# Kernel optimization log

Measured on AMD Instinct MI355X. Metric: run time of the kernel, lower is better.

The kernel has to match this reference:

```python
import jax, jax.numpy as jnp
import numpy as np

DIM = 256
NUM_HEADS = 8
HEAD_DIM = DIM // NUM_HEADS


def setup_inputs() -> dict:
    key = jax.random.key(0)
    k_x, k_wq, k_bq, k_wp, k_bp = jax.random.split(key, 5)
    x = jax.random.normal(k_x, (4, DIM, 64, 64), dtype=jnp.float32)
    # 1x1 convs == per-pixel linear layers over channels
    w_qkv = jax.random.normal(k_wq, (3 * DIM, DIM), dtype=jnp.float32) * (DIM ** -0.5)
    b_qkv = jax.random.normal(k_bq, (3 * DIM,), dtype=jnp.float32) * 0.02
    w_proj = jax.random.normal(k_wp, (DIM, DIM), dtype=jnp.float32) * (DIM ** -0.5)
    b_proj = jax.random.normal(k_bp, (DIM,), dtype=jnp.float32) * 0.02
    return {"x": x, "w_qkv": w_qkv, "b_qkv": b_qkv, "w_proj": w_proj, "b_proj": b_proj}


def reference(x, w_qkv, b_qkv, w_proj, b_proj):
    B, C, H, W = x.shape
    S = H * W
    h, d = NUM_HEADS, HEAD_DIM
    # flatten spatial dims: (B, C, H, W) -> (B, S, C)
    xf = x.reshape(B, C, S).transpose(0, 2, 1)
    # 1x1 conv qkv: (B, S, 3C)
    qkv = xf @ w_qkv.T + b_qkv
    q, k, v = jnp.split(qkv, 3, axis=-1)
    # channel dim splits as (heads, head_dim): (B, S, C) -> (B, h, S, d)
    split = lambda t: t.reshape(B, S, h, d).transpose(0, 2, 1, 3)
    q, k, v = split(q), split(k), split(v)
    scale = d ** -0.5
    attn = jnp.einsum('bhsd,bhtd->bhst', q, k) * scale  # (B, h, S, S)
    attn = jax.nn.softmax(attn, axis=-1)
    out = jnp.einsum('bhst,bhtd->bhsd', attn, v)
    # merge heads: (B, h, S, d) -> (B, S, C)
    out = out.transpose(0, 2, 1, 3).reshape(B, S, C)
    out = out @ w_proj.T + b_proj
    # back to (B, C, H, W)
    return out.transpose(0, 2, 1).reshape(B, C, H, W)
```

## Files before the change

kernel.cpp:

```cpp
#include <hip/hip_runtime.h>


typedef __attribute__((ext_vector_type(8))) short short8;
typedef __attribute__((ext_vector_type(4))) float f4;

__device__ __forceinline__ short f2bs(float f) {
  union { float f; unsigned u; } v; v.f = f;
  unsigned r = v.u + 0x7FFFu + ((v.u >> 16) & 1u);
  return (short)(r >> 16);
}

__device__ __forceinline__ short8 cvt8(f4 a, f4 b) {
  short8 o;
  o[0] = f2bs(a[0]); o[1] = f2bs(a[1]); o[2] = f2bs(a[2]); o[3] = f2bs(a[3]);
  o[4] = f2bs(b[0]); o[5] = f2bs(b[1]); o[6] = f2bs(b[2]); o[7] = f2bs(b[3]);
  return o;
}

__device__ __forceinline__ int pkhu(float lo, float hi) {
  union { float f; unsigned u; } a, b; a.f = lo; b.f = hi;
  return (int)__builtin_amdgcn_perm(b.u + 0x8000u, a.u + 0x8000u, 0x07060302u);
}

__global__ __launch_bounds__(256) void k_qkv(
    const float* __restrict__ x, const float* __restrict__ w,
    const float* __restrict__ bias,
    short* __restrict__ Qr, short* __restrict__ Kq, short* __restrict__ Vt) {
  const int tid = threadIdx.x;
  const int L = tid & 63, wv = tid >> 6;
  const int ln15 = L & 15, quad = L >> 4;
  const int mt = blockIdx.x;
  const int b = mt >> 6;
  const int s0 = (mt & 63) << 6;
  const int j0 = blockIdx.y << 6;
  const int jw = j0 + wv * 16;

  __shared__ __align__(16) short tl[4 * 64 * 16];

  f4 acc[4] = {{0,0,0,0},{0,0,0,0},{0,0,0,0},{0,0,0,0}};
  const float* wb = w + (jw + ln15) * 256 + quad * 8;
  const float* xb = x + b * (256 * 4096) + s0 + ln15;

#pragma unroll 2
  for (int cb = 0; cb < 256; cb += 32) {
    f4 a0 = *(const f4*)(wb + cb);
    f4 a1 = *(const f4*)(wb + cb + 4);
    short8 af = cvt8(a0, a1);
    const float* xc = xb + (cb + quad * 8) * 4096;
#pragma unroll
    for (int sub = 0; sub < 4; ++sub) {
      const float* xs = xc + sub * 16;
      short8 bf;
#pragma unroll
      for (int jj = 0; jj < 8; ++jj) bf[jj] = f2bs(xs[jj * 4096]);
      acc[sub] = __builtin_amdgcn_mfma_f32_16x16x32_bf16(af, bf, acc[sub], 0, 0, 0);
    }
  }

  float bj[4];
#pragma unroll
  for (int r = 0; r < 4; ++r) bj[r] = bias[jw + quad * 4 + r];

  const int type = j0 >> 8;
  if (type == 2) {
    const int jv = jw - 512;
    const int h = jv >> 5;
    const int dbase = jv & 31;
#pragma unroll
    for (int r = 0; r < 4; ++r) {
      const int d = dbase + quad * 4 + r;
      short* vp = Vt + (size_t)((b * 8 + h) * 32 + d) * 4096 + s0 + ln15;
#pragma unroll
      for (int sub = 0; sub < 4; ++sub)
        vp[sub * 16] = f2bs(acc[sub][r] + bj[r]);
    }
  } else {
    const float qsc = 0.17677669529663689f * 1.44269504088896f;
    const float mul = (type == 0) ? qsc : 1.0f;
    short* dst = (type == 0) ? Qr : Kq;
    const int hj = jw & 255;
    short* tw = tl + wv * 1024;
#pragma unroll
    for (int sub = 0; sub < 4; ++sub) {
      const int s = sub * 16 + ln15;
      const int swz = (s >> 2) & 1;
#pragma unroll
      for (int r = 0; r < 4; ++r) {
        const int dl = quad * 4 + r;
        tw[s * 16 + (((dl >> 3) ^ swz) * 8) + (dl & 7)] = f2bs((acc[sub][r] + bj[r]) * mul);
      }
    }
    const int h = hj >> 5;
    const int d0 = hj & 31;
#pragma unroll
    for (int i = 0; i < 2; ++i) {
      const int sl = i * 32 + (L >> 1);
      const int gg = L & 1;
      const int g2 = gg ^ ((sl >> 2) & 1);
      short8 row = *(const short8*)(tw + sl * 16 + g2 * 8);
      *(short8*)(dst + (size_t)((b * 8 + h) * 4096 + s0 + sl) * 32 + d0 + gg * 8) = row;
    }
  }
}

__global__ __launch_bounds__(256, 8) void k_attn(
    const short* __restrict__ Qr, const short* __restrict__ Kq,
    const short* __restrict__ Vt, short* __restrict__ O) {
  const int tid = threadIdx.x;
  const int L = tid & 63, wv = tid >> 6;
  const int ln15 = L & 15, quad = L >> 4;
  const int bh = blockIdx.y;
  const int b = bh >> 3, h = bh & 7;
  const int qt = wv & 1, half = wv >> 1;
  const int qb = blockIdx.x * 64 + qt * 32;

  const short* Qb = Qr + (size_t)bh * 4096 * 32;
  const short* Kb = Kq + (size_t)bh * 4096 * 32 + half * 2048 * 32;
  const short* Vb = Vt + (size_t)bh * 32 * 4096 + half * 2048;

  __shared__ __align__(16) short plds[4][2048];
  __shared__ float l_up[2][32];
  short* pw = plds[wv];
  const int sw = ln15 & 14;

  short8 qf[2];
#pragma unroll
  for (int qs = 0; qs < 2; ++qs)
    qf[qs] = *(const short8*)(Qb + (qb + qs * 16 + ln15) * 32 + quad * 8);

  f4 acc[2][2] = {{{0,0,0,0},{0,0,0,0}},{{0,0,0,0},{0,0,0,0}}};
  float lsum[2] = {0.f, 0.f};
  const f4 z4 = {0.f, 0.f, 0.f, 0.f};

  const short* kp = Kb + ln15 * 32 + quad * 8;
  const short* vp = Vb + ln15 * 4096 + quad * 8;

  for (int kb = 0; kb < 2048; kb += 64) {
#pragma unroll
    for (int t = 0; t < 4; ++t) {
      short8 kf = *(const short8*)(kp + (kb + t * 16) * 32);
#pragma unroll
      for (int qs = 0; qs < 2; ++qs) {
        f4 sc = __builtin_amdgcn_mfma_f32_16x16x32_bf16(kf, qf[qs], z4, 0, 0, 0);
        float p0 = __builtin_amdgcn_exp2f(sc[0]);
        float p1 = __builtin_amdgcn_exp2f(sc[1]);
        float p2 = __builtin_amdgcn_exp2f(sc[2]);
        float p3 = __builtin_amdgcn_exp2f(sc[3]);
        lsum[qs] += (p0 + p1) + (p2 + p3);
        int2 pr;
        pr.x = pkhu(p0, p1);
        pr.y = pkhu(p2, p3);
        const int gw = ((t << 2) + quad) ^ sw;
        *(int2*)(pw + qs * 1024 + ln15 * 64 + gw * 4) = pr;
      }
    }
#pragma unroll
    for (int ks = 0; ks < 2; ++ks) {
      short8 vf0 = *(const short8*)(vp + kb + ks * 32);
      short8 vf1 = *(const short8*)(vp + 16 * 4096 + kb + ks * 32);
#pragma unroll
      for (int qs = 0; qs < 2; ++qs) {
        const int g0 = ((ks << 3) + (quad << 1)) ^ sw;
        short8 pf = *(const short8*)(pw + qs * 1024 + ln15 * 64 + g0 * 4);
        acc[qs][0] = __builtin_amdgcn_mfma_f32_16x16x32_bf16(pf, vf0, acc[qs][0], 0, 0, 0);
        acc[qs][1] = __builtin_amdgcn_mfma_f32_16x16x32_bf16(pf, vf1, acc[qs][1], 0, 0, 0);
      }
    }
  }

  float lfull[2];
#pragma unroll
  for (int qs = 0; qs < 2; ++qs) {
    float l = lsum[qs];
    l += __shfl_xor(l, 16);
    l += __shfl_xor(l, 32);
    lfull[qs] = l;
  }

  if (half == 1) {
    float* cw = (float*)plds[wv];
#pragma unroll
    for (int qs = 0; qs < 2; ++qs) {
#pragma unroll
      for (int dg = 0; dg < 2; ++dg)
#pragma unroll
        for (int r = 0; r < 4; ++r)
          cw[(qs * 16 + quad * 4 + r) * 32 + dg * 16 + ln15] = acc[qs][dg][r];
      if (quad == 0) l_up[qt][qs * 16 + ln15] = lfull[qs];
    }
  }
  __syncthreads();
  if (half == 0) {
    const float* cu = (const float*)plds[wv + 2];
#pragma unroll
    for (int qs = 0; qs < 2; ++qs) {
#pragma unroll
      for (int r = 0; r < 4; ++r) {
        const float lown = __shfl(lfull[qs], quad * 4 + r);
        const float lup = l_up[qt][qs * 16 + quad * 4 + r];
        const float rl = 1.0f / (lown + lup);
        const int sg = qb + qs * 16 + quad * 4 + r;
        short* op = O + (size_t)(b * 4096 + sg) * 256 + h * 32 + ln15;
        const int ci = (qs * 16 + quad * 4 + r) * 32 + ln15;
        op[0]  = f2bs((acc[qs][0][r] + cu[ci]) * rl);
        op[16] = f2bs((acc[qs][1][r] + cu[ci + 16]) * rl);
      }
    }
  }
}

__global__ __launch_bounds__(256) void k_proj(
    const short* __restrict__ O, const float* __restrict__ w,
    const float* __restrict__ bias, float* __restrict__ out) {
  const int tid = threadIdx.x;
  const int L = tid & 63, wv = tid >> 6;
  const int ln15 = L & 15, quad = L >> 4;
  const int m0 = blockIdx.x * 64 + wv * 16;
  const int n0 = blockIdx.y << 6;
  const int b = m0 >> 12, s0 = m0 & 4095;

  f4 acc[4] = {{0,0,0,0},{0,0,0,0},{0,0,0,0},{0,0,0,0}};
  const short* Ob = O + (size_t)(m0 + ln15) * 256 + quad * 8;
  const float* wb = w + (n0 + ln15) * 256 + quad * 8;

#pragma unroll 2
  for (int cb = 0; cb < 256; cb += 32) {
    short8 af = *(const short8*)(Ob + cb);
#pragma unroll
    for (int sub = 0; sub < 4; ++sub) {
      f4 b0 = *(const f4*)(wb + sub * (16 * 256) + cb);
      f4 b1 = *(const f4*)(wb + sub * (16 * 256) + cb + 4);
      short8 bf = cvt8(b0, b1);
      acc[sub] = __builtin_amdgcn_mfma_f32_16x16x32_bf16(af, bf, acc[sub], 0, 0, 0);
    }
  }

  __shared__ float tl[4][64 * 17];
  float* tw = tl[wv];
#pragma unroll
  for (int sub = 0; sub < 4; ++sub) {
    const float bv = bias[n0 + sub * 16 + ln15];
#pragma unroll
    for (int r = 0; r < 4; ++r)
      tw[(sub * 16 + ln15) * 17 + quad * 4 + r] = acc[sub][r] + bv;
  }
#pragma unroll
  for (int i = 0; i < 4; ++i) {
    const int c = i * 16 + (L >> 2);
    const int ms = (L & 3) * 4;
    f4 v;
#pragma unroll
    for (int j = 0; j < 4; ++j) v[j] = tw[c * 17 + ms + j];
    *(f4*)(out + (size_t)b * (256 * 4096) + (size_t)(n0 + c) * 4096 + s0 + ms) = v;
  }
}

extern "C" void kernel_launch(void* const* d_in, const int* in_sizes, int n_in,
                              void* d_out, int out_size, void* d_ws, size_t ws_size,
                              hipStream_t stream) {
  const float* x      = (const float*)d_in[0];
  const float* w_qkv  = (const float*)d_in[1];
  const float* b_qkv  = (const float*)d_in[2];
  const float* w_proj = (const float*)d_in[3];
  const float* b_proj = (const float*)d_in[4];
  float* out = (float*)d_out;

  const size_t SEG = (size_t)4 * 8 * 4096 * 32;
  short* Qr = (short*)d_ws;
  short* Kq = Qr + SEG;
  short* Vt = Kq + SEG;
  short* O  = Vt + SEG;

  k_qkv <<<dim3(256, 12), 256, 0, stream>>>(x, w_qkv, b_qkv, Qr, Kq, Vt);
  k_attn<<<dim3(64, 32),  256, 0, stream>>>(Qr, Kq, Vt, O);
  k_proj<<<dim3(256, 4),  256, 0, stream>>>(O, w_proj, b_proj, out);
}
```

Baseline: 328.0 us.

## Pre-convert weights and transpose x to bf16, prefetch K in attention

Adds two prep kernels: one converts the QKV and projection weights to bf16, the other transposes x into a bf16 (B,S,C) layout through swizzled shared memory. The QKV and projection GEMMs then load contiguous bf16 fragments instead of strided fp32 loads with per-element conversion. The attention loop double-buffers K fragments in registers and lowers launch bounds occupancy from 8 to 6. Epilogues are also rewritten: Q/K are stored directly, V goes through an LDS transpose, and proj writes without LDS. The cost is two extra launches and the O buffer being reused as scratch for the transposed x.

```diff
diff --git a/kernel.cpp b/kernel.cpp
--- a/kernel.cpp
+++ b/kernel.cpp
@@ -10,11 +10,8 @@
   return (short)(r >> 16);
 }
 
-__device__ __forceinline__ short8 cvt8(f4 a, f4 b) {
-  short8 o;
-  o[0] = f2bs(a[0]); o[1] = f2bs(a[1]); o[2] = f2bs(a[2]); o[3] = f2bs(a[3]);
-  o[4] = f2bs(b[0]); o[5] = f2bs(b[1]); o[6] = f2bs(b[2]); o[7] = f2bs(b[3]);
-  return o;
+__device__ __forceinline__ int pkrne(float a, float b) {
+  return (int)((unsigned short)f2bs(a) | ((unsigned)f2bs(b) << 16));
 }
 
 __device__ __forceinline__ int pkhu(float lo, float hi) {
@@ -22,8 +19,47 @@
   return (int)__builtin_amdgcn_perm(b.u + 0x8000u, a.u + 0x8000u, 0x07060302u);
 }
 
+__global__ __launch_bounds__(256) void k_prep_w(
+    const float* __restrict__ wq, const float* __restrict__ wp,
+    short* __restrict__ wqb, short* __restrict__ wpb) {
+  const int i = blockIdx.x * 256 + threadIdx.x;
+  const int NQ = 768 * 256 / 4;
+  f4 v; short* dst; int off;
+  if (i < NQ) { v = ((const f4*)wq)[i]; dst = wqb; off = i * 4; }
+  else        { v = ((const f4*)wp)[i - NQ]; dst = wpb; off = (i - NQ) * 4; }
+  int2 pr; pr.x = pkrne(v[0], v[1]); pr.y = pkrne(v[2], v[3]);
+  *(int2*)(dst + off) = pr;
+}
+
+__global__ __launch_bounds__(256) void k_prep_x(
+    const float* __restrict__ x, short* __restrict__ xT) {
+  const int t = threadIdx.x;
+  const int b = blockIdx.z, c0 = blockIdx.y * 64, s0 = blockIdx.x * 64;
+  __shared__ __align__(16) short tile[64 * 64];
+#pragma unroll
+  for (int pass = 0; pass < 4; ++pass) {
+    const int cl = pass * 16 + (t >> 4);
+    const int sl = (t & 15) * 4;
+    f4 v = *(const f4*)(x + ((size_t)(b * 256 + c0 + cl)) * 4096 + s0 + sl);
+#pragma unroll
+    for (int k = 0; k < 4; ++k) {
+      const int s = sl + k;
+      tile[s * 64 + (cl ^ ((s & 7) << 3))] = f2bs(v[k]);
+    }
+  }
+  __syncthreads();
+#pragma unroll
+  for (int i = 0; i < 2; ++i) {
+    const int s = t >> 2;
+    const int gc = (t & 3) + i * 4;
+    const int gg = gc ^ (s & 7);
+    short8 row = *(const short8*)(tile + s * 64 + gg * 8);
+    *(short8*)(xT + ((size_t)(b * 4096 + s0 + s)) * 256 + c0 + gc * 8) = row;
+  }
+}
+
 __global__ __launch_bounds__(256) void k_qkv(
-    const float* __restrict__ x, const float* __restrict__ w,
+    const short* __restrict__ xT, const short* __restrict__ wqb,
     const float* __restrict__ bias,
     short* __restrict__ Qr, short* __restrict__ Kq, short* __restrict__ Vt) {
   const int tid = threadIdx.x;
@@ -35,75 +71,66 @@
   const int j0 = blockIdx.y << 6;
   const int jw = j0 + wv * 16;
 
-  __shared__ __align__(16) short tl[4 * 64 * 16];
+  __shared__ __align__(16) short tl[4][1024];
 
   f4 acc[4] = {{0,0,0,0},{0,0,0,0},{0,0,0,0},{0,0,0,0}};
-  const float* wb = w + (jw + ln15) * 256 + quad * 8;
-  const float* xb = x + b * (256 * 4096) + s0 + ln15;
-
-#pragma unroll 2
+  const short* wb = wqb + (jw + ln15) * 256 + quad * 8;
+  const short* xb = xT + (size_t)(b * 4096 + s0 + ln15) * 256 + quad * 8;
+
+#pragma unroll
   for (int cb = 0; cb < 256; cb += 32) {
-    f4 a0 = *(const f4*)(wb + cb);
-    f4 a1 = *(const f4*)(wb + cb + 4);
-    short8 af = cvt8(a0, a1);
-    const float* xc = xb + (cb + quad * 8) * 4096;
+    short8 af = *(const short8*)(wb + cb);
 #pragma unroll
     for (int sub = 0; sub < 4; ++sub) {
-      const float* xs = xc + sub * 16;
-      short8 bf;
-#pragma unroll
-      for (int jj = 0; jj < 8; ++jj) bf[jj] = f2bs(xs[jj * 4096]);
-      acc[sub] = __builtin_amdgcn_mfma_f32_16x16x32_bf16(af, bf, acc[sub], 0, 0, 0);
-    }
-  }
-
+      short8 bfr = *(const short8*)(xb + sub * (16 * 256) + cb);
+      acc[sub] = __builtin_amdgcn_mfma_f32_16x16x32_bf16(af, bfr, acc[sub], 0, 0, 0);
+    }
+  }
   float bj[4];
 #pragma unroll
   for (int r = 0; r < 4; ++r) bj[r] = bias[jw + quad * 4 + r];
 
   const int type = j0 >> 8;
-  if (type == 2) {
-    const int jv = jw - 512;
-    const int h = jv >> 5;
-    const int dbase = jv & 31;
-#pragma unroll
-    for (int r = 0; r < 4; ++r) {
-      const int d = dbase + quad * 4 + r;
-      short* vp = Vt + (size_t)((b * 8 + h) * 32 + d) * 4096 + s0 + ln15;
-#pragma unroll
-      for (int sub = 0; sub < 4; ++sub)
-        vp[sub * 16] = f2bs(acc[sub][r] + bj[r]);
-    }
-  } else {
+  const int hj = jw & 255;
+  const int bh = b * 8 + (hj >> 5);
+  const int db = hj & 31;
+
+  if (type != 2) {
     const float qsc = 0.17677669529663689f * 1.44269504088896f;
     const float mul = (type == 0) ? qsc : 1.0f;
     short* dst = (type == 0) ? Qr : Kq;
-    const int hj = jw & 255;
-    short* tw = tl + wv * 1024;
+#pragma unroll
+    for (int sub = 0; sub < 4; ++sub) {
+      float v0 = (acc[sub][0] + bj[0]) * mul;
+      float v1 = (acc[sub][1] + bj[1]) * mul;
+      float v2 = (acc[sub][2] + bj[2]) * mul;
+      float v3 = (acc[sub][3] + bj[3]) * mul;
+      int2 pr; pr.x = pkhu(v0, v1); pr.y = pkhu(v2, v3);
+      *(int2*)(dst + (size_t)(bh * 4096 + s0 + sub * 16 + ln15) * 32 + db + quad * 4) = pr;
+    }
+  } else {
+    short* tv = tl[wv];
 #pragma unroll
     for (int sub = 0; sub < 4; ++sub) {
       const int s = sub * 16 + ln15;
-      const int swz = (s >> 2) & 1;
 #pragma unroll
       for (int r = 0; r < 4; ++r) {
         const int dl = quad * 4 + r;
-        tw[s * 16 + (((dl >> 3) ^ swz) * 8) + (dl & 7)] = f2bs((acc[sub][r] + bj[r]) * mul);
+        tv[dl * 64 + ((((s >> 3) ^ dl) & 7) << 3) + (s & 7)] = f2bs(acc[sub][r] + bj[r]);
       }
     }
-    const int h = hj >> 5;
-    const int d0 = hj & 31;
 #pragma unroll
     for (int i = 0; i < 2; ++i) {
-      const int sl = i * 32 + (L >> 1);
-      const int gg = L & 1;
-      const int g2 = gg ^ ((sl >> 2) & 1);
-      short8 row = *(const short8*)(tw + sl * 16 + g2 * 8);
-      *(short8*)(dst + (size_t)((b * 8 + h) * 4096 + s0 + sl) * 32 + d0 + gg * 8) = row;
-    }
-  }
-}
-
-__global__ __launch_bounds__(256, 8) void k_attn(
+      const int dl = i * 8 + (L >> 3);
+      const int gs = L & 7;
+      const int gg = gs ^ (dl & 7);
+      short8 row = *(const short8*)(tv + dl * 64 + gg * 8);
+      *(short8*)(Vt + (size_t)(bh * 32 + db + dl) * 4096 + s0 + gs * 8) = row;
+    }
+  }
+}
+
+__global__ __launch_bounds__(256, 6) void k_attn(
     const short* __restrict__ Qr, const short* __restrict__ Kq,
     const short* __restrict__ Vt, short* __restrict__ O) {
   const int tid = threadIdx.x;
@@ -135,13 +162,19 @@
   const short* kp = Kb + ln15 * 32 + quad * 8;
   const short* vp = Vb + ln15 * 4096 + quad * 8;
 
-  for (int kb = 0; kb < 2048; kb += 64) {
+  short8 kfA[4], kfB[4];
+#pragma unroll
+  for (int t = 0; t < 4; ++t) kfA[t] = *(const short8*)(kp + t * 16 * 32);
+
+  auto chunk = [&](int kb, short8* kfu, short8* kfn, int knext) {
+#pragma unroll
+    for (int t = 0; t < 4; ++t)
+      kfn[t] = *(const short8*)(kp + (knext + t * 16) * 32);
 #pragma unroll
     for (int t = 0; t < 4; ++t) {
-      short8 kf = *(const short8*)(kp + (kb + t * 16) * 32);
 #pragma unroll
       for (int qs = 0; qs < 2; ++qs) {
-        f4 sc = __builtin_amdgcn_mfma_f32_16x16x32_bf16(kf, qf[qs], z4, 0, 0, 0);
+        f4 sc = __builtin_amdgcn_mfma_f32_16x16x32_bf16(kfu[t], qf[qs], z4, 0, 0, 0);
         float p0 = __builtin_amdgcn_exp2f(sc[0]);
         float p1 = __builtin_amdgcn_exp2f(sc[1]);
         float p2 = __builtin_amdgcn_exp2f(sc[2]);
@@ -166,6 +199,11 @@
         acc[qs][1] = __builtin_amdgcn_mfma_f32_16x16x32_bf16(pf, vf1, acc[qs][1], 0, 0, 0);
       }
     }
+  };
+
+  for (int kb = 0; kb < 2048; kb += 128) {
+    chunk(kb, kfA, kfB, kb + 64);
+    chunk(kb + 64, kfB, kfA, (kb + 128) & 2047);
   }
 
   float lfull[2];
@@ -210,7 +248,7 @@
 }
 
 __global__ __launch_bounds__(256) void k_proj(
-    const short* __restrict__ O, const float* __restrict__ w,
+    const short* __restrict__ O, const short* __restrict__ wpb,
     const float* __restrict__ bias, float* __restrict__ out) {
   const int tid = threadIdx.x;
   const int L = tid & 63, wv = tid >> 6;
@@ -221,37 +259,25 @@
 
   f4 acc[4] = {{0,0,0,0},{0,0,0,0},{0,0,0,0},{0,0,0,0}};
   const short* Ob = O + (size_t)(m0 + ln15) * 256 + quad * 8;
-  const float* wb = w + (n0 + ln15) * 256 + quad * 8;
-
-#pragma unroll 2
+  const short* wb = wpb + (n0 + ln15) * 256 + quad * 8;
+
+#pragma unroll
   for (int cb = 0; cb < 256; cb += 32) {
     short8 af = *(const short8*)(Ob + cb);
 #pragma unroll
     for (int sub = 0; sub < 4; ++sub) {
-      f4 b0 = *(const f4*)(wb + sub * (16 * 256) + cb);
-      f4 b1 = *(const f4*)(wb + sub * (16 * 256) + cb + 4);
-      short8 bf = cvt8(b0, b1);
-      acc[sub] = __builtin_amdgcn_mfma_f32_16x16x32_bf16(af, bf, acc[sub], 0, 0, 0);
-    }
-  }
-
-  __shared__ float tl[4][64 * 17];
-  float* tw = tl[wv];
+      short8 bfr = *(const short8*)(wb + sub * (16 * 256) + cb);
+      acc[sub] = __builtin_amdgcn_mfma_f32_16x16x32_bf16(af, bfr, acc[sub], 0, 0, 0);
+    }
+  }
 #pragma unroll
   for (int sub = 0; sub < 4; ++sub) {
-    const float bv = bias[n0 + sub * 16 + ln15];
-#pragma unroll
-    for (int r = 0; r < 4; ++r)
-      tw[(sub * 16 + ln15) * 17 + quad * 4 + r] = acc[sub][r] + bv;
-  }
-#pragma unroll
-  for (int i = 0; i < 4; ++i) {
-    const int c = i * 16 + (L >> 2);
-    const int ms = (L & 3) * 4;
+    const int c = n0 + sub * 16 + ln15;
+    const float bv = bias[c];
     f4 v;
 #pragma unroll
-    for (int j = 0; j < 4; ++j) v[j] = tw[c * 17 + ms + j];
-    *(f4*)(out + (size_t)b * (256 * 4096) + (size_t)(n0 + c) * 4096 + s0 + ms) = v;
+    for (int r = 0; r < 4; ++r) v[r] = acc[sub][r] + bv;
+    *(f4*)(out + (size_t)b * (256 * 4096) + (size_t)c * 4096 + s0 + quad * 4) = v;
   }
 }
 
@@ -266,12 +292,16 @@
   float* out = (float*)d_out;
 
   const size_t SEG = (size_t)4 * 8 * 4096 * 32;
-  short* Qr = (short*)d_ws;
-  short* Kq = Qr + SEG;
-  short* Vt = Kq + SEG;
-  short* O  = Vt + SEG;
-
-  k_qkv <<<dim3(256, 12), 256, 0, stream>>>(x, w_qkv, b_qkv, Qr, Kq, Vt);
-  k_attn<<<dim3(64, 32),  256, 0, stream>>>(Qr, Kq, Vt, O);
-  k_proj<<<dim3(256, 4),  256, 0, stream>>>(O, w_proj, b_proj, out);
-}
+  short* Qr  = (short*)d_ws;
+  short* Kq  = Qr + SEG;
+  short* Vt  = Kq + SEG;
+  short* OX  = Vt + SEG;
+  short* wqb = OX + SEG;
+  short* wpb = wqb + 768 * 256;
+
+  k_prep_w<<<256, 256, 0, stream>>>(w_qkv, w_proj, wqb, wpb);
+  k_prep_x<<<dim3(64, 4, 4), 256, 0, stream>>>(x, OX);
+  k_qkv <<<dim3(256, 12), 256, 0, stream>>>(OX, wqb, b_qkv, Qr, Kq, Vt);
+  k_attn<<<dim3(64, 32),  256, 0, stream>>>(Qr, Kq, Vt, OX);
+  k_proj<<<dim3(256, 4),  256, 0, stream>>>(OX, wpb, b_proj, out);
+}
```

After: 721.6 us. 2.2x slower.
